# Kernel tuning notes

Hardware: AMD Instinct MI355X
Metric: run time of the kernel (lower is better)

Reference implementation:

```python
import jax, jax.numpy as jnp
import numpy as np

N_POINTS = 2_097_152  # ~1448x1448 sample points
N_CELLS = 5
N_SHAPES = 3 * N_CELLS * N_CELLS  # 75 primitives (tri, circle, ellipse per cell)


def _build_params():
    # Replicates the structure of VectorGraphicsRGB2IntegrandSlang.__init__:
    # per cell: triangle (11 floats), circle (8 floats), ellipse (9 floats).
    rng = np.random.default_rng(42)
    n, jf = N_CELLS, 1.0
    cw = 1.0 / n
    params = []
    for i in range(n):
        for j in range(n):
            bx = (i + 0.5) / n + (rng.random() - 0.5) * jf * cw
            by = (j + 0.5) / n + (rng.random() - 0.5) * jf * cw
            rad = 0.4 / n
            ang = np.sort(rng.random(3) * 2.0 * 3.14159)
            pxs = np.clip(bx + rad * np.cos(ang), 0.0, 1.0)
            pys = np.clip(by + rad * np.sin(ang), 0.0, 1.0)
            params += [1.0, pxs[0], pys[0], pxs[1], pys[1], pxs[2], pys[2], 0.0] + list(rng.random(3))
            cxx = (i + 0.5) / n + (rng.random() - 0.5) * jf * cw
            cyy = (j + 0.5) / n + (rng.random() - 0.5) * jf * cw
            cr = rng.random() * 0.1 / n + 0.05 / n
            cxx = min(max(cxx, cr), 1.0 - cr)
            cyy = min(max(cyy, cr), 1.0 - cr)
            params += [3.0, cxx, cyy, cr, 0.0] + list(rng.random(3))
            exx = (i + 0.5) / n + (rng.random() - 0.5) * jf * cw
            eyy = (j + 0.5) / n + (rng.random() - 0.5) * jf * cw
            erx = rng.random() * 0.12 / n + 0.04 / n
            ery = rng.random() * 0.12 / n + 0.04 / n
            exx = min(max(exx, erx), 1.0 - erx)
            eyy = min(max(eyy, ery), 1.0 - ery)
            params += [2.0, exx, eyy, erx, ery, 0.0] + list(rng.random(3))
    return np.asarray(params, dtype=np.float32)  # [700]


def setup_inputs() -> dict:
    key = jax.random.key(0)
    k1, _ = jax.random.split(key)
    x = jax.random.uniform(k1, (N_POINTS, 2), dtype=jnp.float32)  # points in [0,1]^2
    p = jnp.asarray(_build_params())
    return {"x": x, "p": p}


def reference(x, p):
    # Parse the fixed-layout parameter vector: 25 cells x 28 floats.
    cells = p.reshape(N_CELLS * N_CELLS, 28)
    tri, circ, ell = cells[:, :11], cells[:, 11:19], cells[:, 19:]
    px, py = x[:, 0:1], x[:, 1:2]  # [N,1] broadcast against [25] shapes

    # Triangle containment: consistent sign of the three edge cross products.
    ax, ay, bx, by, cx, cy = (tri[:, k] for k in range(1, 7))
    e0 = (px - ax) * (by - ay) - (py - ay) * (bx - ax)  # [N,25]
    e1 = (px - bx) * (cy - by) - (py - by) * (cx - bx)
    e2 = (px - cx) * (ay - cy) - (py - cy) * (ax - cx)
    tri_in = ((e0 >= 0) & (e1 >= 0) & (e2 >= 0)) | ((e0 <= 0) & (e1 <= 0) & (e2 <= 0))

    # Circle containment.
    ocx, ocy, orr = circ[:, 1], circ[:, 2], circ[:, 3]
    circ_in = (px - ocx) ** 2 + (py - ocy) ** 2 <= orr ** 2

    # Ellipse containment.
    ecx, ecy, erx, ery = ell[:, 1], ell[:, 2], ell[:, 3], ell[:, 4]
    ell_in = ((px - ecx) / erx) ** 2 + ((py - ecy) / ery) ** 2 <= 1.0

    # Interleave per-cell in shader evaluation order: triangle, circle, ellipse.
    inside = jnp.stack([tri_in, circ_in, ell_in], axis=2).reshape(x.shape[0], N_SHAPES)
    colors = jnp.stack([tri[:, 8:11], circ[:, 5:8], ell[:, 6:9]], axis=1).reshape(N_SHAPES, 3)

    last = (N_SHAPES - 1) - jnp.argmax(inside[:, ::-1], axis=1)  # [N]
    any_in = inside.any(axis=1)
    return jnp.where(any_in[:, None], colors[last], jnp.zeros((), x.dtype))  # [N,3]
```

## Files before the change

kernel.cpp:

```cpp
#include <hip/hip_runtime.h>

#pragma clang fp contract(off)

#define NPTS 2097152
#define PPT  8
#define NTHREADS (NPTS / PPT)

#define L_COL  980
#define LDS_FLOATS (980 + 304)

#define EPS_T 1e-6f
#define EPS_C 1e-7f
#define EPS_E 1e-5f

__device__ __noinline__ int exact_point(float px, float py, int ihi, int jhi,
                                        const float* __restrict__ p) {
    int idx = -1;
#pragma clang loop unroll(disable)
    for (int s = 0; s < 4; ++s) {
        int gi = ihi + (s >> 1), gj = jhi + (s & 1);
        if (gi < 1 || gi > 5 || gj < 1 || gj > 5) continue;
        int c = 5 * (gi - 1) + (gj - 1);
        const float* cell = p + 28 * c;
        float ax = cell[1], ay = cell[2], bx = cell[3], by = cell[4], cx = cell[5], cy = cell[6];
        float e0 = (px - ax) * (by - ay) - (py - ay) * (bx - ax);
        float e1 = (px - bx) * (cy - by) - (py - by) * (cx - bx);
        float e2 = (px - cx) * (ay - cy) - (py - cy) * (ax - cx);
        bool tin = (e0 >= 0.f && e1 >= 0.f && e2 >= 0.f) ||
                   (e0 <= 0.f && e1 <= 0.f && e2 <= 0.f);
        if (tin) idx = 3 * c;
        float dx = px - cell[12], dy = py - cell[13];
        if (dx * dx + dy * dy <= cell[14] * cell[14]) idx = 3 * c + 1;
        float u = (px - cell[20]) / cell[22];
        float v = (py - cell[21]) / cell[23];
        if (u * u + v * v <= 1.0f) idx = 3 * c + 2;
    }
    return idx;
}

__global__ __launch_bounds__(256) void vg_fused(const float* __restrict__ x,
                                                const float* __restrict__ p,
                                                float* __restrict__ out) {
    __shared__ float lds[LDS_FLOATS];
    int tl = threadIdx.x;
    int t  = blockIdx.x * 256 + tl;

    if (tl < 49) {
        int gi = tl / 7, gj = tl % 7;
        float* o = lds + tl * 20;
        if (gi >= 1 && gi <= 5 && gj >= 1 && gj <= 5) {
            int c = (gi - 1) * 5 + (gj - 1);
            const float* cell = p + c * 28;
            float ax = cell[1], ay = cell[2], bx = cell[3], by = cell[4], cx = cell[5], cy = cell[6];
            float d0y = by - ay, d0x = bx - ax;
            float d1y = cy - by, d1x = cx - bx;
            float d2y = ay - cy, d2x = ax - cx;
            o[0] = d0y; o[1] = -d0x; o[2] = (float)((double)ay * (double)d0x - (double)ax * (double)d0y);
            o[3] = d1y; o[4] = -d1x; o[5] = (float)((double)by * (double)d1x - (double)bx * (double)d1y);
            o[6] = d2y; o[7] = -d2x; o[8] = (float)((double)cy * (double)d2x - (double)cx * (double)d2y);
            o[9]  = cell[12]; o[10] = cell[13]; o[11] = cell[14] * cell[14];
            o[12] = cell[20]; o[13] = cell[21]; o[14] = 1.0f / cell[22]; o[15] = 1.0f / cell[23];
        } else {
            o[0] = 0.f; o[1] = 0.f; o[2] = 10.f;
            o[3] = 0.f; o[4] = 0.f; o[5] = -10.f;
            o[6] = 0.f; o[7] = 0.f; o[8] = 0.f;
            o[9] = 0.f; o[10] = 0.f; o[11] = -10.f;
            o[12] = 1000.f; o[13] = 1000.f; o[14] = 1.f; o[15] = 1.f;
        }
        o[16] = 0.f; o[17] = 0.f; o[18] = 0.f; o[19] = 0.f;
    }
    if (tl >= 128 && tl < 204) {
        int e = tl - 128;
        float* col = lds + L_COL + e * 4;
        if (e < 75) {
            int c = e / 3, kind = e - 3 * c;
            const float* cell = p + c * 28;
            int base = (kind == 0) ? 8 : (kind == 1) ? 16 : 25;
            col[0] = cell[base]; col[1] = cell[base + 1]; col[2] = cell[base + 2];
        } else {
            col[0] = 0.f; col[1] = 0.f; col[2] = 0.f;
        }
        col[3] = 0.f;
    }
    __syncthreads();

    const float4* x4 = (const float4*)x;
    float PX[PPT], PY[PPT];
    int idx[PPT], ihi[PPT], jhi[PPT];
    bool unc[PPT];
#pragma unroll
    for (int k = 0; k < PPT; k += 2) {
        float4 v = x4[4 * t + k / 2];
        PX[k] = v.x; PY[k] = v.y; PX[k + 1] = v.z; PY[k + 1] = v.w;
    }
#pragma unroll
    for (int k = 0; k < PPT; ++k) {
        idx[k] = -1; unc[k] = false;
        ihi[k] = (int)floorf(__builtin_fmaf(PX[k], 5.0f, 0.4025f));
        jhi[k] = (int)floorf(__builtin_fmaf(PY[k], 5.0f, 0.4025f));
    }

#pragma unroll
    for (int a = 0; a < 2; ++a) {
#pragma unroll
        for (int b = 0; b < 2; ++b) {
#pragma unroll
            for (int k = 0; k < PPT; ++k) {
                int gi = ihi[k] + a, gj = jhi[k] + b;
                const float4* c4 = (const float4*)(lds + (gi * 7 + gj) * 20);
                float4 q0 = c4[0], q1 = c4[1], q2 = c4[2], q3 = c4[3];
                float X = PX[k], Y = PY[k];

                float e0 = __builtin_fmaf(X, q0.x, __builtin_fmaf(Y, q0.y, q0.z));
                float e1 = __builtin_fmaf(X, q0.w, __builtin_fmaf(Y, q1.x, q1.y));
                float e2 = __builtin_fmaf(X, q1.z, __builtin_fmaf(Y, q1.w, q2.x));
                float lo = __builtin_fminf(__builtin_fminf(e0, e1), e2);
                float hi = __builtin_fmaxf(__builtin_fmaxf(e0, e1), e2);
                bool ts = (lo >= EPS_T) || (hi <= -EPS_T);
                bool tr = (lo >= -EPS_T) || (hi <= EPS_T);
                unc[k] = unc[k] || (ts != tr);
                int sid = 15 * gi + 3 * gj - 18;
                idx[k] = ts ? sid : idx[k];

                float dx = X - q2.y, dy = Y - q2.z;
                float tc = __builtin_fmaf(dx, dx, dy * dy);
                unc[k] = unc[k] || (__builtin_fabsf(tc - q2.w) < EPS_C);
                idx[k] = (tc <= q2.w) ? sid + 1 : idx[k];

                float ex = X - q3.x, ey = Y - q3.y;
                float u = ex * q3.z, v = ey * q3.w;
                float te = __builtin_fmaf(u, u, v * v);
                unc[k] = unc[k] || (__builtin_fabsf(te - 1.0f) < EPS_E);
                idx[k] = (te <= 1.0f) ? sid + 2 : idx[k];
            }
        }
    }

#pragma unroll
    for (int k = 0; k < PPT; ++k)
        if (__builtin_expect(unc[k], 0))
            idx[k] = exact_point(PX[k], PY[k], ihi[k], jhi[k], p);

    const float4* col4 = (const float4*)(lds + L_COL);
    float4 C[PPT];
#pragma unroll
    for (int k = 0; k < PPT; ++k) C[k] = col4[idx[k] < 0 ? 75 : idx[k]];

    float4* out4 = (float4*)out;
#pragma unroll
    for (int k = 0; k < PPT; k += 4) {
        int o = 6 * t + 3 * (k / 4);
        out4[o + 0] = make_float4(C[k].x, C[k].y, C[k].z, C[k + 1].x);
        out4[o + 1] = make_float4(C[k + 1].y, C[k + 1].z, C[k + 2].x, C[k + 2].y);
        out4[o + 2] = make_float4(C[k + 2].z, C[k + 3].x, C[k + 3].y, C[k + 3].z);
    }
}

extern "C" void kernel_launch(void* const* d_in, const int* in_sizes, int n_in,
                              void* d_out, int out_size, void* d_ws, size_t ws_size,
                              hipStream_t stream) {
    const float* x = (const float*)d_in[0];
    const float* p = (const float*)d_in[1];
    float* out = (float*)d_out;
    (void)d_ws; (void)ws_size;

    vg_fused<<<NTHREADS / 256, 256, 0, stream>>>(x, p, out);
}
```

Measured before the change: 91.62 us.

## Skip non-overlapping neighbor cells per point and halve points per thread

Each point now tests only the candidate cells whose shapes can reach it, using the fractional position in the cell to rule out the lower or left neighbor, instead of always testing four cells. The padded 7x7 LDS table with sentinel cells is replaced by a compact 5x5 table with explicit bounds checks. Points per thread drop from 8 to 4, doubling the thread count. The test is now a branch, so lanes that take different paths can diverge, and the 0.8055 cutoff must stay conservative for correctness.

```diff
diff --git a/kernel.cpp b/kernel.cpp
--- a/kernel.cpp
+++ b/kernel.cpp
@@ -3,24 +3,24 @@
 #pragma clang fp contract(off)
 
 #define NPTS 2097152
-#define PPT  8
+#define PPT  4
 #define NTHREADS (NPTS / PPT)
 
-#define L_COL  980
-#define LDS_FLOATS (980 + 304)
+#define L_COL  500
+#define LDS_FLOATS (500 + 304)
 
 #define EPS_T 1e-6f
 #define EPS_C 1e-7f
 #define EPS_E 1e-5f
 
-__device__ __noinline__ int exact_point(float px, float py, int ihi, int jhi,
+__device__ __noinline__ int exact_point(float px, float py, int ih, int jh,
                                         const float* __restrict__ p) {
     int idx = -1;
 #pragma clang loop unroll(disable)
     for (int s = 0; s < 4; ++s) {
-        int gi = ihi + (s >> 1), gj = jhi + (s & 1);
-        if (gi < 1 || gi > 5 || gj < 1 || gj > 5) continue;
-        int c = 5 * (gi - 1) + (gj - 1);
+        int ii = ih - 1 + (s >> 1), jj = jh - 1 + (s & 1);
+        if ((unsigned)ii > 4u || (unsigned)jj > 4u) continue;
+        int c = 5 * ii + jj;
         const float* cell = p + 28 * c;
         float ax = cell[1], ay = cell[2], bx = cell[3], by = cell[4], cx = cell[5], cy = cell[6];
         float e0 = (px - ax) * (by - ay) - (py - ay) * (bx - ax);
@@ -45,28 +45,18 @@
     int tl = threadIdx.x;
     int t  = blockIdx.x * 256 + tl;
 
-    if (tl < 49) {
-        int gi = tl / 7, gj = tl % 7;
+    if (tl < 25) {
+        const float* cell = p + tl * 28;
         float* o = lds + tl * 20;
-        if (gi >= 1 && gi <= 5 && gj >= 1 && gj <= 5) {
-            int c = (gi - 1) * 5 + (gj - 1);
-            const float* cell = p + c * 28;
-            float ax = cell[1], ay = cell[2], bx = cell[3], by = cell[4], cx = cell[5], cy = cell[6];
-            float d0y = by - ay, d0x = bx - ax;
-            float d1y = cy - by, d1x = cx - bx;
-            float d2y = ay - cy, d2x = ax - cx;
-            o[0] = d0y; o[1] = -d0x; o[2] = (float)((double)ay * (double)d0x - (double)ax * (double)d0y);
-            o[3] = d1y; o[4] = -d1x; o[5] = (float)((double)by * (double)d1x - (double)bx * (double)d1y);
-            o[6] = d2y; o[7] = -d2x; o[8] = (float)((double)cy * (double)d2x - (double)cx * (double)d2y);
-            o[9]  = cell[12]; o[10] = cell[13]; o[11] = cell[14] * cell[14];
-            o[12] = cell[20]; o[13] = cell[21]; o[14] = 1.0f / cell[22]; o[15] = 1.0f / cell[23];
-        } else {
-            o[0] = 0.f; o[1] = 0.f; o[2] = 10.f;
-            o[3] = 0.f; o[4] = 0.f; o[5] = -10.f;
-            o[6] = 0.f; o[7] = 0.f; o[8] = 0.f;
-            o[9] = 0.f; o[10] = 0.f; o[11] = -10.f;
-            o[12] = 1000.f; o[13] = 1000.f; o[14] = 1.f; o[15] = 1.f;
-        }
+        float ax = cell[1], ay = cell[2], bx = cell[3], by = cell[4], cx = cell[5], cy = cell[6];
+        float d0y = by - ay, d0x = bx - ax;
+        float d1y = cy - by, d1x = cx - bx;
+        float d2y = ay - cy, d2x = ax - cx;
+        o[0] = d0y; o[1] = -d0x; o[2] = (float)((double)ay * (double)d0x - (double)ax * (double)d0y);
+        o[3] = d1y; o[4] = -d1x; o[5] = (float)((double)by * (double)d1x - (double)bx * (double)d1y);
+        o[6] = d2y; o[7] = -d2x; o[8] = (float)((double)cy * (double)d2x - (double)cx * (double)d2y);
+        o[9]  = cell[12]; o[10] = cell[13]; o[11] = cell[14] * cell[14];
+        o[12] = cell[20]; o[13] = cell[21]; o[14] = 1.0f / cell[22]; o[15] = 1.0f / cell[23];
         o[16] = 0.f; o[17] = 0.f; o[18] = 0.f; o[19] = 0.f;
     }
     if (tl >= 128 && tl < 204) {
@@ -85,19 +75,21 @@
     __syncthreads();
 
     const float4* x4 = (const float4*)x;
-    float PX[PPT], PY[PPT];
-    int idx[PPT], ihi[PPT], jhi[PPT];
-    bool unc[PPT];
-#pragma unroll
-    for (int k = 0; k < PPT; k += 2) {
-        float4 v = x4[4 * t + k / 2];
-        PX[k] = v.x; PY[k] = v.y; PX[k + 1] = v.z; PY[k + 1] = v.w;
-    }
+    float4 xa = x4[2 * t], xb = x4[2 * t + 1];
+    float PX[PPT] = {xa.x, xa.z, xb.x, xb.z};
+    float PY[PPT] = {xa.y, xa.w, xb.y, xb.w};
+    int idx[PPT], ih[PPT], jh[PPT];
+    bool nxL[PPT], nyL[PPT], unc[PPT];
+
 #pragma unroll
     for (int k = 0; k < PPT; ++k) {
         idx[k] = -1; unc[k] = false;
-        ihi[k] = (int)floorf(__builtin_fmaf(PX[k], 5.0f, 0.4025f));
-        jhi[k] = (int)floorf(__builtin_fmaf(PY[k], 5.0f, 0.4025f));
+        float vx = __builtin_fmaf(PX[k], 5.0f, 0.4025f);
+        float vy = __builtin_fmaf(PY[k], 5.0f, 0.4025f);
+        float fx = floorf(vx), fy = floorf(vy);
+        ih[k] = (int)fx; jh[k] = (int)fy;
+        nxL[k] = (vx - fx) <= 0.8055f;
+        nyL[k] = (vy - fy) <= 0.8055f;
     }
 
 #pragma unroll
@@ -106,32 +98,37 @@
         for (int b = 0; b < 2; ++b) {
 #pragma unroll
             for (int k = 0; k < PPT; ++k) {
-                int gi = ihi[k] + a, gj = jhi[k] + b;
-                const float4* c4 = (const float4*)(lds + (gi * 7 + gj) * 20);
-                float4 q0 = c4[0], q1 = c4[1], q2 = c4[2], q3 = c4[3];
-                float X = PX[k], Y = PY[k];
+                int ii = ih[k] + a - 1, jj = jh[k] + b - 1;
+                bool act = ((a == 1) | nxL[k]) & ((b == 1) | nyL[k]) &
+                           ((unsigned)ii <= 4u) & ((unsigned)jj <= 4u);
+                if (act) {
+                    int ci = 5 * ii + jj;
+                    const float4* c4 = (const float4*)(lds + ci * 20);
+                    float4 q0 = c4[0], q1 = c4[1], q2 = c4[2], q3 = c4[3];
+                    float X = PX[k], Y = PY[k];
 
-                float e0 = __builtin_fmaf(X, q0.x, __builtin_fmaf(Y, q0.y, q0.z));
-                float e1 = __builtin_fmaf(X, q0.w, __builtin_fmaf(Y, q1.x, q1.y));
-                float e2 = __builtin_fmaf(X, q1.z, __builtin_fmaf(Y, q1.w, q2.x));
-                float lo = __builtin_fminf(__builtin_fminf(e0, e1), e2);
-                float hi = __builtin_fmaxf(__builtin_fmaxf(e0, e1), e2);
-                bool ts = (lo >= EPS_T) || (hi <= -EPS_T);
-                bool tr = (lo >= -EPS_T) || (hi <= EPS_T);
-                unc[k] = unc[k] || (ts != tr);
-                int sid = 15 * gi + 3 * gj - 18;
-                idx[k] = ts ? sid : idx[k];
+                    float e0 = __builtin_fmaf(X, q0.x, __builtin_fmaf(Y, q0.y, q0.z));
+                    float e1 = __builtin_fmaf(X, q0.w, __builtin_fmaf(Y, q1.x, q1.y));
+                    float e2 = __builtin_fmaf(X, q1.z, __builtin_fmaf(Y, q1.w, q2.x));
+                    float lo = __builtin_fminf(__builtin_fminf(e0, e1), e2);
+                    float hi = __builtin_fmaxf(__builtin_fmaxf(e0, e1), e2);
+                    bool ts = (lo >= EPS_T) || (hi <= -EPS_T);
+                    bool tr = (lo >= -EPS_T) || (hi <= EPS_T);
+                    unc[k] = unc[k] || (ts != tr);
+                    int sid = 3 * ci;
+                    idx[k] = ts ? sid : idx[k];
 
-                float dx = X - q2.y, dy = Y - q2.z;
-                float tc = __builtin_fmaf(dx, dx, dy * dy);
-                unc[k] = unc[k] || (__builtin_fabsf(tc - q2.w) < EPS_C);
-                idx[k] = (tc <= q2.w) ? sid + 1 : idx[k];
+                    float dx = X - q2.y, dy = Y - q2.z;
+                    float tc = __builtin_fmaf(dx, dx, dy * dy);
+                    unc[k] = unc[k] || (__builtin_fabsf(tc - q2.w) < EPS_C);
+                    idx[k] = (tc <= q2.w) ? sid + 1 : idx[k];
 
-                float ex = X - q3.x, ey = Y - q3.y;
-                float u = ex * q3.z, v = ey * q3.w;
-                float te = __builtin_fmaf(u, u, v * v);
-                unc[k] = unc[k] || (__builtin_fabsf(te - 1.0f) < EPS_E);
-                idx[k] = (te <= 1.0f) ? sid + 2 : idx[k];
+                    float ex = X - q3.x, ey = Y - q3.y;
+                    float u = ex * q3.z, v = ey * q3.w;
+                    float te = __builtin_fmaf(u, u, v * v);
+                    unc[k] = unc[k] || (__builtin_fabsf(te - 1.0f) < EPS_E);
+                    idx[k] = (te <= 1.0f) ? sid + 2 : idx[k];
+                }
             }
         }
     }
@@ -139,21 +136,18 @@
 #pragma unroll
     for (int k = 0; k < PPT; ++k)
         if (__builtin_expect(unc[k], 0))
-            idx[k] = exact_point(PX[k], PY[k], ihi[k], jhi[k], p);
+            idx[k] = exact_point(PX[k], PY[k], ih[k], jh[k], p);
 
     const float4* col4 = (const float4*)(lds + L_COL);
-    float4 C[PPT];
-#pragma unroll
-    for (int k = 0; k < PPT; ++k) C[k] = col4[idx[k] < 0 ? 75 : idx[k]];
+    float4 c0 = col4[idx[0] < 0 ? 75 : idx[0]];
+    float4 c1 = col4[idx[1] < 0 ? 75 : idx[1]];
+    float4 c2 = col4[idx[2] < 0 ? 75 : idx[2]];
+    float4 c3 = col4[idx[3] < 0 ? 75 : idx[3]];
 
     float4* out4 = (float4*)out;
-#pragma unroll
-    for (int k = 0; k < PPT; k += 4) {
-        int o = 6 * t + 3 * (k / 4);
-        out4[o + 0] = make_float4(C[k].x, C[k].y, C[k].z, C[k + 1].x);
-        out4[o + 1] = make_float4(C[k + 1].y, C[k + 1].z, C[k + 2].x, C[k + 2].y);
-        out4[o + 2] = make_float4(C[k + 2].z, C[k + 3].x, C[k + 3].y, C[k + 3].z);
-    }
+    out4[3 * t + 0] = make_float4(c0.x, c0.y, c0.z, c1.x);
+    out4[3 * t + 1] = make_float4(c1.y, c1.z, c2.x, c2.y);
+    out4[3 * t + 2] = make_float4(c2.z, c3.x, c3.y, c3.z);
 }
 
 extern "C" void kernel_launch(void* const* d_in, const int* in_sizes, int n_in,
```

Measured after the change: 80.75 us. 11.9% less time.

## Process two points per thread with batched LDS loads and float2 stores

Applied to the files above, without the earlier changes.

Cuts points per thread from 8 to 2, launching four times as many threads with fewer registers each. The loop now handles one point at a time and loads all four neighbouring cells' parameters from LDS up front. The output is written as three float2 stores instead of float4 stores. The goal is more occupancy and latency hiding, in exchange for more blocks each repeating the LDS table setup, and narrower, less coalesced global stores.

```diff
diff --git a/kernel.cpp b/kernel.cpp
--- a/kernel.cpp
+++ b/kernel.cpp
@@ -3,7 +3,7 @@
 #pragma clang fp contract(off)
 
 #define NPTS 2097152
-#define PPT  8
+#define PPT  2
 #define NTHREADS (NPTS / PPT)
 
 #define L_COL  980
@@ -13,14 +13,14 @@
 #define EPS_C 1e-7f
 #define EPS_E 1e-5f
 
-__device__ __noinline__ int exact_point(float px, float py, int ihi, int jhi,
+__device__ __noinline__ int exact_point(float px, float py, int ih, int jh,
                                         const float* __restrict__ p) {
     int idx = -1;
 #pragma clang loop unroll(disable)
     for (int s = 0; s < 4; ++s) {
-        int gi = ihi + (s >> 1), gj = jhi + (s & 1);
-        if (gi < 1 || gi > 5 || gj < 1 || gj > 5) continue;
-        int c = 5 * (gi - 1) + (gj - 1);
+        int ii = ih - 1 + (s >> 1), jj = jh - 1 + (s & 1);
+        if ((unsigned)ii > 4u || (unsigned)jj > 4u) continue;
+        int c = 5 * ii + jj;
         const float* cell = p + 28 * c;
         float ax = cell[1], ay = cell[2], bx = cell[3], by = cell[4], cx = cell[5], cy = cell[6];
         float e0 = (px - ax) * (by - ay) - (py - ay) * (bx - ax);
@@ -84,76 +84,72 @@
     }
     __syncthreads();
 
-    const float4* x4 = (const float4*)x;
-    float PX[PPT], PY[PPT];
-    int idx[PPT], ihi[PPT], jhi[PPT];
+    float4 xv = ((const float4*)x)[t];
+    float PX[PPT] = {xv.x, xv.z};
+    float PY[PPT] = {xv.y, xv.w};
+    int idx[PPT], ih[PPT], jh[PPT];
     bool unc[PPT];
-#pragma unroll
-    for (int k = 0; k < PPT; k += 2) {
-        float4 v = x4[4 * t + k / 2];
-        PX[k] = v.x; PY[k] = v.y; PX[k + 1] = v.z; PY[k + 1] = v.w;
-    }
+
 #pragma unroll
     for (int k = 0; k < PPT; ++k) {
+        ih[k] = (int)floorf(__builtin_fmaf(PX[k], 5.0f, 0.4025f));
+        jh[k] = (int)floorf(__builtin_fmaf(PY[k], 5.0f, 0.4025f));
         idx[k] = -1; unc[k] = false;
-        ihi[k] = (int)floorf(__builtin_fmaf(PX[k], 5.0f, 0.4025f));
-        jhi[k] = (int)floorf(__builtin_fmaf(PY[k], 5.0f, 0.4025f));
     }
 
 #pragma unroll
-    for (int a = 0; a < 2; ++a) {
+    for (int k = 0; k < PPT; ++k) {
+        float X = PX[k], Y = PY[k];
+        const float* base = lds + (7 * ih[k] + jh[k]) * 20;
+        float4 Q[4][4];
 #pragma unroll
-        for (int b = 0; b < 2; ++b) {
+        for (int s = 0; s < 4; ++s) {
+            const float4* c4 = (const float4*)(base + ((s >> 1) * 140 + (s & 1) * 20));
+            Q[s][0] = c4[0]; Q[s][1] = c4[1]; Q[s][2] = c4[2]; Q[s][3] = c4[3];
+        }
+
 #pragma unroll
-            for (int k = 0; k < PPT; ++k) {
-                int gi = ihi[k] + a, gj = jhi[k] + b;
-                const float4* c4 = (const float4*)(lds + (gi * 7 + gj) * 20);
-                float4 q0 = c4[0], q1 = c4[1], q2 = c4[2], q3 = c4[3];
-                float X = PX[k], Y = PY[k];
+        for (int s = 0; s < 4; ++s) {
+            float4 q0 = Q[s][0], q1 = Q[s][1], q2 = Q[s][2], q3 = Q[s][3];
+            int gi = ih[k] + (s >> 1), gj = jh[k] + (s & 1);
+            int sid = 15 * gi + 3 * gj - 18;
 
-                float e0 = __builtin_fmaf(X, q0.x, __builtin_fmaf(Y, q0.y, q0.z));
-                float e1 = __builtin_fmaf(X, q0.w, __builtin_fmaf(Y, q1.x, q1.y));
-                float e2 = __builtin_fmaf(X, q1.z, __builtin_fmaf(Y, q1.w, q2.x));
-                float lo = __builtin_fminf(__builtin_fminf(e0, e1), e2);
-                float hi = __builtin_fmaxf(__builtin_fmaxf(e0, e1), e2);
-                bool ts = (lo >= EPS_T) || (hi <= -EPS_T);
-                bool tr = (lo >= -EPS_T) || (hi <= EPS_T);
-                unc[k] = unc[k] || (ts != tr);
-                int sid = 15 * gi + 3 * gj - 18;
-                idx[k] = ts ? sid : idx[k];
+            float e0 = __builtin_fmaf(X, q0.x, __builtin_fmaf(Y, q0.y, q0.z));
+            float e1 = __builtin_fmaf(X, q0.w, __builtin_fmaf(Y, q1.x, q1.y));
+            float e2 = __builtin_fmaf(X, q1.z, __builtin_fmaf(Y, q1.w, q2.x));
+            float lo = __builtin_fminf(__builtin_fminf(e0, e1), e2);
+            float hi = __builtin_fmaxf(__builtin_fmaxf(e0, e1), e2);
+            bool ts = (lo >= EPS_T) || (hi <= -EPS_T);
+            bool tr = (lo >= -EPS_T) || (hi <= EPS_T);
+            unc[k] = unc[k] | (ts != tr);
+            idx[k] = ts ? sid : idx[k];
 
-                float dx = X - q2.y, dy = Y - q2.z;
-                float tc = __builtin_fmaf(dx, dx, dy * dy);
-                unc[k] = unc[k] || (__builtin_fabsf(tc - q2.w) < EPS_C);
-                idx[k] = (tc <= q2.w) ? sid + 1 : idx[k];
+            float dx = X - q2.y, dy = Y - q2.z;
+            float tc = __builtin_fmaf(dx, dx, dy * dy);
+            unc[k] = unc[k] | (__builtin_fabsf(tc - q2.w) < EPS_C);
+            idx[k] = (tc <= q2.w) ? sid + 1 : idx[k];
 
-                float ex = X - q3.x, ey = Y - q3.y;
-                float u = ex * q3.z, v = ey * q3.w;
-                float te = __builtin_fmaf(u, u, v * v);
-                unc[k] = unc[k] || (__builtin_fabsf(te - 1.0f) < EPS_E);
-                idx[k] = (te <= 1.0f) ? sid + 2 : idx[k];
-            }
+            float ex = X - q3.x, ey = Y - q3.y;
+            float u = ex * q3.z, v = ey * q3.w;
+            float te = __builtin_fmaf(u, u, v * v);
+            unc[k] = unc[k] | (__builtin_fabsf(te - 1.0f) < EPS_E);
+            idx[k] = (te <= 1.0f) ? sid + 2 : idx[k];
         }
     }
 
 #pragma unroll
     for (int k = 0; k < PPT; ++k)
         if (__builtin_expect(unc[k], 0))
-            idx[k] = exact_point(PX[k], PY[k], ihi[k], jhi[k], p);
+            idx[k] = exact_point(PX[k], PY[k], ih[k], jh[k], p);
 
     const float4* col4 = (const float4*)(lds + L_COL);
-    float4 C[PPT];
-#pragma unroll
-    for (int k = 0; k < PPT; ++k) C[k] = col4[idx[k] < 0 ? 75 : idx[k]];
+    float4 c0 = col4[idx[0] < 0 ? 75 : idx[0]];
+    float4 c1 = col4[idx[1] < 0 ? 75 : idx[1]];
 
-    float4* out4 = (float4*)out;
-#pragma unroll
-    for (int k = 0; k < PPT; k += 4) {
-        int o = 6 * t + 3 * (k / 4);
-        out4[o + 0] = make_float4(C[k].x, C[k].y, C[k].z, C[k + 1].x);
-        out4[o + 1] = make_float4(C[k + 1].y, C[k + 1].z, C[k + 2].x, C[k + 2].y);
-        out4[o + 2] = make_float4(C[k + 2].z, C[k + 3].x, C[k + 3].y, C[k + 3].z);
-    }
+    float2* o2 = (float2*)out;
+    o2[3 * t + 0] = make_float2(c0.x, c0.y);
+    o2[3 * t + 1] = make_float2(c0.z, c1.x);
+    o2[3 * t + 2] = make_float2(c1.y, c1.z);
 }
 
 extern "C" void kernel_launch(void* const* d_in, const int* in_sizes, int n_in,
```

Result: faster. 80.40 us (-12.3%).
